# Optimization experiments

Measured on AMD Instinct MI355X. Metric: run time of the kernel, lower is better.

The kernel has to match this reference:

```python
import jax, jax.numpy as jnp
import numpy as np

N_HEADS = 4
SIGMA = 6.0
T_IN = 12
T_TOTAL = 24


def setup_inputs() -> dict:
    key = jax.random.key(0)
    k1, k2, k3, k4, k5 = jax.random.split(key, 5)
    B, T, N, C, K = 16, T_IN, 5000, 4, 16
    x = jax.random.normal(k1, (B, T, N, C), dtype=jnp.float32)
    dists = jax.random.uniform(k2, (N, K), dtype=jnp.float32) * 10.0  # kNN distances
    neighbors = jax.random.randint(k3, (N, K), 0, N)                  # kNN indices
    d_in = T * N_HEADS                   # 48
    d_out = T_TOTAL - T_IN               # 12
    W = jax.random.normal(k4, (d_in, d_out), dtype=jnp.float32) * (1.0 / np.sqrt(d_in))
    b = jax.random.normal(k5, (d_out,), dtype=jnp.float32) * 0.01
    return {"x": x, "dists": dists, "W": W, "b": b, "neighbors": neighbors}


def reference(x, dists, W, b, neighbors):
    B, T, N, C = x.shape
    H = N_HEADS
    # lambda_h = h/H for h = 1..H
    lam = jnp.arange(1, H + 1, dtype=x.dtype) / H                     # [H]
    # weights[n,k,h] = exp(-d_{nk}^2 * lam_h / sigma^2)
    w = jnp.exp(-(dists ** 2)[:, :, None] * lam / (SIGMA ** 2))       # [N,K,H]
    # gather neighbor features: [B,T,N,K,C]
    xg = x[:, :, neighbors, :]
    # distance-weighted aggregation over neighbors -> [B,T,N,H,C]
    agg = jnp.einsum('btnkc,nkh->btnhc', xg, w)
    # permute (0,2,4,1,3) -> [B,N,C,T,H], flatten last two -> [B,N,C,T*H]
    feat = jnp.transpose(agg, (0, 2, 4, 1, 3)).reshape(B, N, C, T * H)
    # shrink: Linear + ReLU -> [B,N,C,T_TOTAL-T]
    y = jax.nn.relu(feat @ W + b)
    # -> [B, T_TOTAL-T, N, C]
    y = jnp.transpose(y, (0, 3, 1, 2))
    return jnp.concatenate([x, y], axis=1)                            # [B,T_TOTAL,N,C]
```

## Files before the change

kernel.cpp:

```cpp
#include <hip/hip_runtime.h>

#define Bz 16
#define Tin 12
#define Ttot 24
#define NN 5000
#define Cc 4
#define KK 16
#define HH 4
#define OO 12
#define TH 48
#define BT 192
#define G  8
#define JJ 24

#define K1_NB 64
#define K1_BT 24

__global__ __launch_bounds__(256) void transpose_concat_kernel(
    const float4* __restrict__ x4,
    float4* __restrict__ xT2,
    float4* __restrict__ out4)
{
    __shared__ float4 tile[K1_BT][K1_NB + 1];
    const int n0  = blockIdx.x * K1_NB;
    const int g   = blockIdx.y;
    const int bt0 = g * K1_BT;
    const int rem = min(K1_NB, NN - n0);
    const int tid = threadIdx.x;

    #pragma unroll
    for (int r = 0; r < (K1_NB * K1_BT) / 256; r++) {
        int tau = r * 256 + tid;
        int j = tau / K1_NB;
        int i = tau % K1_NB;
        if (i < rem) {
            int bt = bt0 + j;
            float4 v = x4[(size_t)bt * NN + n0 + i];
            tile[j][i] = v;
            int b = bt / Tin, t = bt - b * Tin;
            out4[(size_t)(b * Ttot + t) * NN + n0 + i] = v;
        }
    }
    __syncthreads();

    #pragma unroll
    for (int r = 0; r < (K1_NB * K1_BT) / 256; r++) {
        int tau = r * 256 + tid;
        int i = tau / K1_BT;
        int j = tau - i * K1_BT;
        if (i < rem) {
            xT2[((size_t)g * NN + (n0 + i)) * JJ + j] = tile[j][i];
        }
    }
}

#define NPB 8
#define FST 5
#define FSB 61
#define FSN 123

__global__ __launch_bounds__(192) void gnn_main_kernel(
    const float4* __restrict__ xT2,
    const float* __restrict__ dists,
    const float* __restrict__ W,
    const float* __restrict__ bias,
    const int*   __restrict__ nbrs,
    float4* __restrict__ out4)
{
    __shared__ float4 feat[NPB * FSN];
    __shared__ float4 w4_s[NPB][KK];
    __shared__ float  W_s[TH * OO];
    __shared__ float  bias_s[OO];
    __shared__ int    nbr_s[NPB][KK];

    const int bid = blockIdx.x;
    const int g   = bid & 7;
    const int n0  = (bid >> 3) * NPB;
    const int tid = threadIdx.x;

    for (int i = tid; i < TH * OO; i += 192) W_s[i] = W[i];
    if (tid < OO) bias_s[tid] = bias[tid];
    if (tid < NPB * KK) {
        int nl = tid >> 4, k = tid & 15;
        nbr_s[nl][k] = nbrs[(n0 + nl) * KK + k];
        float d = dists[(n0 + nl) * KK + k];
        float e = -(d * d) * (1.0f / 144.0f);
        float4 wv;
        wv.x = expf(e);
        wv.y = expf(2.0f * e);
        wv.z = expf(3.0f * e);
        wv.w = expf(4.0f * e);
        w4_s[nl][k] = wv;
    }
    __syncthreads();

    {
        const int nl  = tid / JJ;
        const int j   = tid - nl * JJ;
        const int b_l = j / Tin;
        const int t   = j - b_l * Tin;
        const float4* xg = xT2 + (size_t)g * NN * JJ;

        float4 a0 = {0,0,0,0}, a1 = {0,0,0,0}, a2 = {0,0,0,0}, a3 = {0,0,0,0};
        #pragma unroll
        for (int k = 0; k < KK; k++) {
            float4 xv = xg[(size_t)nbr_s[nl][k] * JJ + j];
            float4 wv = w4_s[nl][k];
            a0.x += wv.x * xv.x; a0.y += wv.x * xv.y; a0.z += wv.x * xv.z; a0.w += wv.x * xv.w;
            a1.x += wv.y * xv.x; a1.y += wv.y * xv.y; a1.z += wv.y * xv.z; a1.w += wv.y * xv.w;
            a2.x += wv.z * xv.x; a2.y += wv.z * xv.y; a2.z += wv.z * xv.z; a2.w += wv.z * xv.w;
            a3.x += wv.w * xv.x; a3.y += wv.w * xv.y; a3.z += wv.w * xv.z; a3.w += wv.w * xv.w;
        }
        const int base = nl * FSN + b_l * FSB + t * FST;
        feat[base + 0] = a0;
        feat[base + 1] = a1;
        feat[base + 2] = a2;
        feat[base + 3] = a3;
    }
    __syncthreads();

    {
        const int nl  = tid & 7;
        const int bo  = tid >> 3;
        const int b_l = bo / OO;
        const int o   = bo - b_l * OO;
        const float bz = bias_s[o];
        float4 acc = {bz, bz, bz, bz};
        const int fbase = nl * FSN + b_l * FSB;
        #pragma unroll
        for (int t = 0; t < Tin; t++) {
            #pragma unroll
            for (int h = 0; h < HH; h++) {
                float  wv = W_s[(t * HH + h) * OO + o];
                float4 f  = feat[fbase + t * FST + h];
                acc.x += wv * f.x; acc.y += wv * f.y;
                acc.z += wv * f.z; acc.w += wv * f.w;
            }
        }
        acc.x = fmaxf(acc.x, 0.0f); acc.y = fmaxf(acc.y, 0.0f);
        acc.z = fmaxf(acc.z, 0.0f); acc.w = fmaxf(acc.w, 0.0f);
        const int b = g * 2 + b_l;
        out4[(size_t)(b * Ttot + Tin + o) * NN + n0 + nl] = acc;
    }
}

extern "C" void kernel_launch(void* const* d_in, const int* in_sizes, int n_in,
                              void* d_out, int out_size, void* d_ws, size_t ws_size,
                              hipStream_t stream) {
    const float* x     = (const float*)d_in[0];
    const float* dists = (const float*)d_in[1];
    const float* W     = (const float*)d_in[2];
    const float* bias  = (const float*)d_in[3];
    const int*   nbrs  = (const int*)d_in[4];
    float4* out4 = (float4*)d_out;
    float4* xT2  = (float4*)d_ws;

    dim3 g1((NN + K1_NB - 1) / K1_NB, G);
    hipLaunchKernelGGL(transpose_concat_kernel, g1, dim3(256), 0, stream,
                       (const float4*)x, xT2, out4);

    hipLaunchKernelGGL(gnn_main_kernel, dim3((NN / NPB) * G), dim3(192), 0, stream,
                       (const float4*)xT2, dists, W, bias, nbrs, out4);
}
```

Baseline: 104.8 us.

## Move input passthrough copy into main kernel and use nontemporal output stores

The copy of x into the first half of the output moves from the transpose kernel into the main kernel, where each block copies its own slice while the weights are computed. The transpose kernel now only writes the workspace. Output stores use nontemporal hints so they do not push the gathered workspace out of cache. The transpose grid is also flattened, interleaving groups so neighbouring blocks share tiles. Total traffic is the same, but the main kernel now carries extra global loads and stores before its first barrier.

```diff
diff --git a/kernel.cpp b/kernel.cpp
--- a/kernel.cpp
+++ b/kernel.cpp
@@ -9,21 +9,26 @@
 #define HH 4
 #define OO 12
 #define TH 48
-#define BT 192
 #define G  8
 #define JJ 24
+
+typedef float f32x4 __attribute__((ext_vector_type(4)));
+__device__ __forceinline__ void nt_store4(float4* p, float4 v) {
+    f32x4 t; t.x = v.x; t.y = v.y; t.z = v.z; t.w = v.w;
+    __builtin_nontemporal_store(t, (f32x4*)p);
+}
 
 #define K1_NB 64
 #define K1_BT 24
 
-__global__ __launch_bounds__(256) void transpose_concat_kernel(
+__global__ __launch_bounds__(256) void transpose_kernel(
     const float4* __restrict__ x4,
-    float4* __restrict__ xT2,
-    float4* __restrict__ out4)
+    float4* __restrict__ xT2)
 {
     __shared__ float4 tile[K1_BT][K1_NB + 1];
-    const int n0  = blockIdx.x * K1_NB;
-    const int g   = blockIdx.y;
+    const int bid = blockIdx.x;
+    const int g   = bid & 7;
+    const int n0  = (bid >> 3) * K1_NB;
     const int bt0 = g * K1_BT;
     const int rem = min(K1_NB, NN - n0);
     const int tid = threadIdx.x;
@@ -33,13 +38,8 @@
         int tau = r * 256 + tid;
         int j = tau / K1_NB;
         int i = tau % K1_NB;
-        if (i < rem) {
-            int bt = bt0 + j;
-            float4 v = x4[(size_t)bt * NN + n0 + i];
-            tile[j][i] = v;
-            int b = bt / Tin, t = bt - b * Tin;
-            out4[(size_t)(b * Ttot + t) * NN + n0 + i] = v;
-        }
+        if (i < rem)
+            tile[j][i] = x4[(size_t)(bt0 + j) * NN + n0 + i];
     }
     __syncthreads();
 
@@ -48,9 +48,8 @@
         int tau = r * 256 + tid;
         int i = tau / K1_BT;
         int j = tau - i * K1_BT;
-        if (i < rem) {
-            xT2[((size_t)g * NN + (n0 + i)) * JJ + j] = tile[j][i];
-        }
+        if (i < rem)
+            xT2[((size_t)g * NN + n0 + i) * JJ + j] = tile[j][i];
     }
 }
 
@@ -60,6 +59,7 @@
 #define FSN 123
 
 __global__ __launch_bounds__(192) void gnn_main_kernel(
+    const float4* __restrict__ x4,
     const float4* __restrict__ xT2,
     const float* __restrict__ dists,
     const float* __restrict__ W,
@@ -91,6 +91,15 @@
         wv.z = expf(3.0f * e);
         wv.w = expf(4.0f * e);
         w4_s[nl][k] = wv;
+    }
+
+    {
+        const int j  = tid >> 3;
+        const int nl = tid & 7;
+        const int bt = g * JJ + j;
+        const int b  = bt / Tin, t = bt - b * Tin;
+        float4 v = x4[(size_t)bt * NN + n0 + nl];
+        nt_store4(&out4[(size_t)(b * Ttot + t) * NN + n0 + nl], v);
     }
     __syncthreads();
 
@@ -140,7 +149,7 @@
         acc.x = fmaxf(acc.x, 0.0f); acc.y = fmaxf(acc.y, 0.0f);
         acc.z = fmaxf(acc.z, 0.0f); acc.w = fmaxf(acc.w, 0.0f);
         const int b = g * 2 + b_l;
-        out4[(size_t)(b * Ttot + Tin + o) * NN + n0 + nl] = acc;
+        nt_store4(&out4[(size_t)(b * Ttot + Tin + o) * NN + n0 + nl], acc);
     }
 }
 
@@ -155,10 +164,11 @@
     float4* out4 = (float4*)d_out;
     float4* xT2  = (float4*)d_ws;
 
-    dim3 g1((NN + K1_NB - 1) / K1_NB, G);
-    hipLaunchKernelGGL(transpose_concat_kernel, g1, dim3(256), 0, stream,
-                       (const float4*)x, xT2, out4);
+    const int ntiles = (NN + K1_NB - 1) / K1_NB;
+    hipLaunchKernelGGL(transpose_kernel, dim3(ntiles * G), dim3(256), 0, stream,
+                       (const float4*)x, xT2);
 
     hipLaunchKernelGGL(gnn_main_kernel, dim3((NN / NPB) * G), dim3(192), 0, stream,
-                       (const float4*)xT2, dists, W, bias, nbrs, out4);
+                       (const float4*)x, (const float4*)xT2,
+                       dists, W, bias, nbrs, out4);
 }
```

Measured after the change: 106.1 us. No clear change (+1.2%).
